# Performance work log

Hardware: AMD Instinct MI355X
Metric: run time of the kernel (lower is better)

Reference implementation:

```python
import jax, jax.numpy as jnp
import numpy as np

N = 50000
E = 800000
EPS = 1e-16
NEG_SLOPE = 0.2

def setup_inputs() -> dict:
    key = jax.random.key(0)
    ks = jax.random.split(key, 10)
    s = lambda fan: 1.0 / np.sqrt(fan)
    return {
        "x": jax.random.normal(ks[0], (N, 128), dtype=jnp.float32),
        "edge_index": jax.random.randint(ks[1], (2, E), 0, N, dtype=jnp.int64),
        "W1": jax.random.normal(ks[2], (128, 4 * 32), dtype=jnp.float32) * s(128),
        "att_src1": jax.random.normal(ks[3], (4, 32), dtype=jnp.float32) * s(32),
        "att_dst1": jax.random.normal(ks[4], (4, 32), dtype=jnp.float32) * s(32),
        "b1": jnp.zeros((128,), dtype=jnp.float32),
        "W2": jax.random.normal(ks[5], (128, 2), dtype=jnp.float32) * s(128),
        "att_src2": jax.random.normal(ks[6], (1, 2), dtype=jnp.float32) * s(2),
        "att_dst2": jax.random.normal(ks[7], (1, 2), dtype=jnp.float32) * s(2),
        "b2": jnp.zeros((2,), dtype=jnp.float32),
    }

def _gat_conv(x, src, dst, W, att_src, att_dst, bias, heads, out_ch, concat):
    n = x.shape[0]
    h = (x @ W).reshape(n, heads, out_ch)                      # [N,H,C]
    a_src = jnp.sum(h * att_src[None], axis=-1)                # [N,H]
    a_dst = jnp.sum(h * att_dst[None], axis=-1)                # [N,H]
    e = jax.nn.leaky_relu(a_src[src] + a_dst[dst], NEG_SLOPE)  # [Etot,H]
    # segment softmax over incoming edges per destination node
    m = jax.ops.segment_max(e, dst, num_segments=n)            # [N,H]
    m = jnp.where(jnp.isfinite(m), m, 0.0)
    ex = jnp.exp(e - m[dst])
    denom = jax.ops.segment_sum(ex, dst, num_segments=n)       # [N,H]
    alpha = ex / (denom[dst] + EPS)                            # [Etot,H]
    out = jax.ops.segment_sum(alpha[:, :, None] * h[src], dst, num_segments=n)  # [N,H,C]
    if concat:
        out = out.reshape(n, heads * out_ch)
    else:
        out = out.mean(axis=1)
    return out + bias

def reference(x, edge_index, W1, att_src1, att_dst1, b1, W2, att_src2, att_dst2, b2):
    n = x.shape[0]
    # PyG GATConv adds self-loops by default
    loops = jnp.arange(n, dtype=edge_index.dtype)
    src = jnp.concatenate([edge_index[0], loops])
    dst = jnp.concatenate([edge_index[1], loops])
    # dropout is identity at inference
    h = jax.nn.elu(_gat_conv(x, src, dst, W1, att_src1, att_dst1, b1, 4, 32, True))
    h = _gat_conv(h, src, dst, W2, att_src2, att_dst2, b2, 1, 2, False)
    return jax.nn.log_softmax(h, axis=1)
```

## Files before the change

### kernel.cpp

```cpp
#include <hip/hip_runtime.h>
#include <hip/hip_bf16.h>

#define NN 50000
#define EE 800000
#define CAP 64
#define CSTRIDE 16
#define NEG_SLOPE 0.2f
#define EPSF 1e-16f
#define BUILD_BLOCKS 4096
#define GEMM_BLOCKS ((NN + 63) / 64)
#define NPAIRS (EE / 2)

typedef unsigned int uint32;
typedef __attribute__((ext_vector_type(8))) short short8;
typedef __attribute__((ext_vector_type(4))) float floatx4;

__device__ __forceinline__ unsigned short f2bf(float f) {
  unsigned int u = __float_as_uint(f);
  unsigned int r = (u + 0x7fffu + ((u >> 16) & 1u)) >> 16;
  return (unsigned short)r;
}
__device__ __forceinline__ float bf_lo(uint32 v) { return __uint_as_float(v << 16); }
__device__ __forceinline__ float bf_hi(uint32 v) { return __uint_as_float(v & 0xffff0000u); }

__device__ __forceinline__ void do_build(int b, const int* __restrict__ ei,
                                         int* __restrict__ counts,
                                         int* __restrict__ csr) {
  const int range = b & 7;
  const int lo = range * (NN / 8);
  const int hi = lo + (NN / 8);
  const int group = b >> 3;
  const int tid0 = group * 256 + threadIdx.x;
  const int stride = (BUILD_BLOCKS >> 3) * 256;

  {
    int n = lo + tid0;
    if (n < hi) csr[n * CAP] = n;
  }

  const int2* __restrict__ dst2 = (const int2*)(ei + EE);
  const int2* __restrict__ src2 = (const int2*)(ei);
  for (int p = tid0; p < NPAIRS; p += stride) {
    int2 d2 = dst2[p];
    int2 s2 = src2[p];
    if (d2.x >= lo && d2.x < hi) {
      int r = atomicAdd(&counts[d2.x * CSTRIDE], 1);
      if (r < CAP) csr[d2.x * CAP + r] = s2.x;
    }
    if (d2.y >= lo && d2.y < hi) {
      int r = atomicAdd(&counts[d2.y * CSTRIDE], 1);
      if (r < CAP) csr[d2.y * CAP + r] = s2.y;
    }
  }
}

__device__ __forceinline__ void do_gemm_tile(
    int tile, const float* __restrict__ x, const unsigned short* __restrict__ Wt,
    const float* __restrict__ att_src1, const float* __restrict__ att_dst1,
    uint32* __restrict__ h1b, float* __restrict__ as1, float* __restrict__ ad1) {
  const int t    = threadIdx.x;
  const int wave = t >> 6;
  const int lane = t & 63;
  const int quad = lane >> 4;
  const int col  = lane & 15;
  const int nodeBase = tile * 64 + wave * 16;

  floatx4 acc[8];
  #pragma unroll
  for (int i = 0; i < 8; i++) acc[i] = (floatx4){0.f, 0.f, 0.f, 0.f};

  int mread = nodeBase + col; if (mread >= NN) mread = NN - 1;
  const float* __restrict__ xrow = x + (size_t)mread * 128 + quad * 8;
  const unsigned short* __restrict__ bbase = Wt + col * 128 + quad * 8;

  #pragma unroll
  for (int ks = 0; ks < 4; ks++) {
    float4 a0 = *(const float4*)(xrow + ks * 32);
    float4 a1 = *(const float4*)(xrow + ks * 32 + 4);
    union { short8 v; unsigned short u[8]; } af;
    af.u[0] = f2bf(a0.x); af.u[1] = f2bf(a0.y);
    af.u[2] = f2bf(a0.z); af.u[3] = f2bf(a0.w);
    af.u[4] = f2bf(a1.x); af.u[5] = f2bf(a1.y);
    af.u[6] = f2bf(a1.z); af.u[7] = f2bf(a1.w);
    #pragma unroll
    for (int tt = 0; tt < 8; tt++) {
      short8 bf = *(const short8*)(bbase + tt * 16 * 128 + ks * 32);
      acc[tt] = __builtin_amdgcn_mfma_f32_16x16x32_bf16(af.v, bf, acc[tt], 0, 0, 0);
    }
  }

  float asv[8], adv[8];
  #pragma unroll
  for (int tt = 0; tt < 8; tt++) {
    asv[tt] = att_src1[tt * 16 + col];
    adv[tt] = att_dst1[tt * 16 + col];
  }

  #pragma unroll
  for (int r = 0; r < 4; r++) {
    const int gn = nodeBase + quad * 4 + r;
    const bool live = (gn < NN);
    #pragma unroll
    for (int tt = 0; tt < 8; tt++) {
      float v = acc[tt][r];
      float w = __shfl_xor(v, 1, 64);
      if (live && ((col & 1) == 0)) {
        uint32 pk = (uint32)f2bf(v) | ((uint32)f2bf(w) << 16);
        h1b[(size_t)gn * 64 + tt * 8 + (col >> 1)] = pk;
      }
    }
    #pragma unroll
    for (int h = 0; h < 4; h++) {
      float ps = acc[2 * h][r] * asv[2 * h] + acc[2 * h + 1][r] * asv[2 * h + 1];
      float pd = acc[2 * h][r] * adv[2 * h] + acc[2 * h + 1][r] * adv[2 * h + 1];
      #pragma unroll
      for (int off = 1; off < 16; off <<= 1) {
        ps += __shfl_xor(ps, off, 64);
        pd += __shfl_xor(pd, off, 64);
      }
      if (live && col == 0) {
        as1[gn * 4 + h] = ps;
        ad1[gn * 4 + h] = pd;
      }
    }
  }
}

__global__ __launch_bounds__(256) void prep_zero_k(
    const float* __restrict__ W1, unsigned short* __restrict__ Wt,
    int* __restrict__ counts) {
  const int step = gridDim.x * 256;
  const int t0 = blockIdx.x * 256 + threadIdx.x;
  for (int i = t0; i < NN * CSTRIDE; i += step)
    counts[i] = ((i & (CSTRIDE - 1)) == 0) ? 1 : 0;
  for (int i = t0; i < 128 * 128; i += step) {
    int k = i >> 7, c = i & 127;
    Wt[c * 128 + k] = f2bf(W1[i]);
  }
}

__global__ __launch_bounds__(256) void work_k(
    const int* __restrict__ ei, int* __restrict__ counts, int* __restrict__ csr,
    const float* __restrict__ x, const unsigned short* __restrict__ Wt,
    const float* __restrict__ att_src1, const float* __restrict__ att_dst1,
    uint32* __restrict__ h1b, float* __restrict__ as1, float* __restrict__ ad1) {
  const int b = blockIdx.x;
  if (b < BUILD_BLOCKS) {
    do_build(b, ei, counts, csr);
  } else {
    do_gemm_tile(b - BUILD_BLOCKS, x, Wt, att_src1, att_dst1, h1b, as1, ad1);
  }
}

__global__ __launch_bounds__(256) void agg1_k(
    const int* __restrict__ counts, const int* __restrict__ csr,
    const uint32* __restrict__ h1b, const float* __restrict__ as1,
    const float* __restrict__ ad1, const float* __restrict__ b1,
    const float* __restrict__ W2, const float* __restrict__ att_src2,
    const float* __restrict__ att_dst2, float4* __restrict__ rec) {
  __shared__ float part[2][3][64];
  const int lane = threadIdx.x & 63;
  const int wv   = threadIdx.x >> 6;
  const int nl   = wv >> 1;
  const int w    = wv & 1;
  const int hd   = lane >> 4;
  const int n = __builtin_amdgcn_readfirstlane(blockIdx.x * 2 + nl);

  int cnt = counts[n * CSTRIDE];
  cnt = __builtin_amdgcn_readfirstlane(cnt < CAP ? cnt : CAP);
  const int half = (cnt + 1) >> 1;
  const int jbeg = w ? half : 0;
  const int jend = w ? cnt : half;
  const int* __restrict__ row = csr + n * CAP;
  const float adv = ad1[n * 4 + hd];

  float den = 0.f, accx = 0.f, accy = 0.f;
  int j = jbeg;
  for (; j + 3 < jend; j += 4) {
    int s0 = row[j], s1 = row[j + 1], s2 = row[j + 2], s3 = row[j + 3];
    float e0 = as1[s0 * 4 + hd] + adv;
    float e1 = as1[s1 * 4 + hd] + adv;
    float e2 = as1[s2 * 4 + hd] + adv;
    float e3 = as1[s3 * 4 + hd] + adv;
    uint32 v0 = h1b[s0 * 64 + lane];
    uint32 v1 = h1b[s1 * 64 + lane];
    uint32 v2 = h1b[s2 * 64 + lane];
    uint32 v3 = h1b[s3 * 64 + lane];
    e0 = (e0 > 0.f) ? e0 : NEG_SLOPE * e0;
    e1 = (e1 > 0.f) ? e1 : NEG_SLOPE * e1;
    e2 = (e2 > 0.f) ? e2 : NEG_SLOPE * e2;
    e3 = (e3 > 0.f) ? e3 : NEG_SLOPE * e3;
    float x0 = __expf(e0), x1 = __expf(e1), x2 = __expf(e2), x3 = __expf(e3);
    den += (x0 + x1) + (x2 + x3);
    accx = fmaf(x0, bf_lo(v0), accx);
    accy = fmaf(x0, bf_hi(v0), accy);
    accx = fmaf(x1, bf_lo(v1), accx);
    accy = fmaf(x1, bf_hi(v1), accy);
    accx = fmaf(x2, bf_lo(v2), accx);
    accy = fmaf(x2, bf_hi(v2), accy);
    accx = fmaf(x3, bf_lo(v3), accx);
    accy = fmaf(x3, bf_hi(v3), accy);
  }
  for (; j < jend; j++) {
    int s = row[j];
    float e = as1[s * 4 + hd] + adv;
    e = (e > 0.f) ? e : NEG_SLOPE * e;
    float ex = __expf(e);
    uint32 v = h1b[s * 64 + lane];
    den += ex;
    accx = fmaf(ex, bf_lo(v), accx);
    accy = fmaf(ex, bf_hi(v), accy);
  }

  if (w == 1) {
    part[nl][0][lane] = den;
    part[nl][1][lane] = accx;
    part[nl][2][lane] = accy;
  }
  __syncthreads();
  if (w == 1) return;
  den  += part[nl][0][lane];
  accx += part[nl][1][lane];
  accy += part[nl][2][lane];

  float inv = 1.f / (den + EPSF);
  float2 bb = ((const float2*)b1)[lane];
  float ox = accx * inv + bb.x;
  float oy = accy * inv + bb.y;
  ox = (ox > 0.f) ? ox : (__expf(ox) - 1.f);
  oy = (oy > 0.f) ? oy : (__expf(oy) - 1.f);

  float4 wq = ((const float4*)W2)[lane];
  float p0 = ox * wq.x + oy * wq.z;
  float p1 = ox * wq.y + oy * wq.w;
  #pragma unroll
  for (int off = 32; off; off >>= 1) {
    p0 += __shfl_xor(p0, off, 64);
    p1 += __shfl_xor(p1, off, 64);
  }
  if (lane == 0) {
    rec[n] = make_float4(p0, p1,
                         p0 * att_src2[0] + p1 * att_src2[1],
                         p0 * att_dst2[0] + p1 * att_dst2[1]);
  }
}

__global__ __launch_bounds__(256) void agg2_k(
    const int* __restrict__ counts, const int* __restrict__ csr,
    const float4* __restrict__ rec, const float* __restrict__ b2,
    float* __restrict__ out) {
  int i = blockIdx.x * 256 + threadIdx.x;
  if (i >= NN * 8) return;
  int n = i >> 3;
  int sub = i & 7;
  const float adv = rec[n].w;
  int cnt = counts[n * CSTRIDE];
  cnt = cnt < CAP ? cnt : CAP;
  const int* __restrict__ row = csr + n * CAP;

  float den = 0.f, a0 = 0.f, a1 = 0.f;
  for (int j = sub; j < cnt; j += 8) {
    int s = row[j];
    float4 rs = rec[s];
    float e = rs.z + adv;
    e = (e > 0.f) ? e : NEG_SLOPE * e;
    float ex = __expf(e);
    den += ex;
    a0 = fmaf(ex, rs.x, a0);
    a1 = fmaf(ex, rs.y, a1);
  }
  #pragma unroll
  for (int off = 4; off; off >>= 1) {
    den += __shfl_down(den, off, 8);
    a0  += __shfl_down(a0, off, 8);
    a1  += __shfl_down(a1, off, 8);
  }
  if (sub == 0) {
    float inv = 1.f / (den + EPSF);
    float o0 = a0 * inv + b2[0];
    float o1 = a1 * inv + b2[1];
    float mx = fmaxf(o0, o1);
    float lse = mx + __logf(__expf(o0 - mx) + __expf(o1 - mx));
    *(float2*)&out[n * 2] = make_float2(o0 - lse, o1 - lse);
  }
}

extern "C" void kernel_launch(void* const* d_in, const int* in_sizes, int n_in,
                              void* d_out, int out_size, void* d_ws, size_t ws_size,
                              hipStream_t stream) {
  const float* x        = (const float*)d_in[0];
  const int*   ei       = (const int*)d_in[1];
  const float* W1       = (const float*)d_in[2];
  const float* att_src1 = (const float*)d_in[3];
  const float* att_dst1 = (const float*)d_in[4];
  const float* b1       = (const float*)d_in[5];
  const float* W2       = (const float*)d_in[6];
  const float* att_src2 = (const float*)d_in[7];
  const float* att_dst2 = (const float*)d_in[8];
  const float* b2       = (const float*)d_in[9];
  float* out = (float*)d_out;

  char* p = (char*)d_ws;
  auto alloc = [&](size_t bytes) {
    char* r = p;
    p += (bytes + 255) & ~size_t(255);
    return r;
  };
  uint32* h1b  = (uint32*)alloc(sizeof(uint32) * NN * 64);
  float* as1   = (float*)alloc(sizeof(float) * NN * 4);
  float* ad1   = (float*)alloc(sizeof(float) * NN * 4);
  float4* rec  = (float4*)alloc(sizeof(float4) * NN);
  int*   counts = (int*)alloc(sizeof(int) * NN * CSTRIDE);
  int*   csr   = (int*)alloc(sizeof(int) * NN * CAP);
  unsigned short* Wt = (unsigned short*)alloc(sizeof(unsigned short) * 128 * 128);

  prep_zero_k<<<512, 256, 0, stream>>>(W1, Wt, counts);
  work_k<<<BUILD_BLOCKS + GEMM_BLOCKS, 256, 0, stream>>>(
      ei, counts, csr, x, Wt, att_src1, att_dst1, h1b, as1, ad1);
  agg1_k<<<NN / 2, 256, 0, stream>>>(counts, csr, h1b, as1, ad1, b1, W2,
                                     att_src2, att_dst2, rec);
  agg2_k<<<(NN * 8 + 255) / 256, 256, 0, stream>>>(counts, csr, rec, b2, out);
}
```

Baseline: 208.1 us.

## Split fused build/GEMM kernel and use one wave per node in aggregation

The combined work kernel that ran CSR build blocks and GEMM tiles side by side is split into two separate launches, so the two jobs no longer overlap. The layer-1 aggregation now gives each node a single wave instead of splitting its edges across two waves with a shared-memory reduction and block barrier. This drops the LDS traffic and __syncthreads and halves the waves per node, but it serialises the build and GEMM phases, adds a launch, and lengthens each wave's edge loop.

```diff
diff --git a/kernel.cpp b/kernel.cpp
--- a/kernel.cpp
+++ b/kernel.cpp
@@ -23,9 +23,23 @@
 __device__ __forceinline__ float bf_lo(uint32 v) { return __uint_as_float(v << 16); }
 __device__ __forceinline__ float bf_hi(uint32 v) { return __uint_as_float(v & 0xffff0000u); }
 
-__device__ __forceinline__ void do_build(int b, const int* __restrict__ ei,
-                                         int* __restrict__ counts,
-                                         int* __restrict__ csr) {
+__global__ __launch_bounds__(256) void prep_zero_k(
+    const float* __restrict__ W1, unsigned short* __restrict__ Wt,
+    int* __restrict__ counts) {
+  const int step = gridDim.x * 256;
+  const int t0 = blockIdx.x * 256 + threadIdx.x;
+  for (int i = t0; i < NN * CSTRIDE; i += step)
+    counts[i] = ((i & (CSTRIDE - 1)) == 0) ? 1 : 0;
+  for (int i = t0; i < 128 * 128; i += step) {
+    int k = i >> 7, c = i & 127;
+    Wt[c * 128 + k] = f2bf(W1[i]);
+  }
+}
+
+__global__ __launch_bounds__(256) void build_k(
+    const int* __restrict__ ei, int* __restrict__ counts,
+    int* __restrict__ csr) {
+  const int b = blockIdx.x;
   const int range = b & 7;
   const int lo = range * (NN / 8);
   const int hi = lo + (NN / 8);
@@ -54,10 +68,11 @@
   }
 }
 
-__device__ __forceinline__ void do_gemm_tile(
-    int tile, const float* __restrict__ x, const unsigned short* __restrict__ Wt,
+__global__ __launch_bounds__(256) void gemm_k(
+    const float* __restrict__ x, const unsigned short* __restrict__ Wt,
     const float* __restrict__ att_src1, const float* __restrict__ att_dst1,
     uint32* __restrict__ h1b, float* __restrict__ as1, float* __restrict__ ad1) {
+  const int tile = blockIdx.x;
   const int t    = threadIdx.x;
   const int wave = t >> 6;
   const int lane = t & 63;
@@ -126,57 +141,25 @@
   }
 }
 
-__global__ __launch_bounds__(256) void prep_zero_k(
-    const float* __restrict__ W1, unsigned short* __restrict__ Wt,
-    int* __restrict__ counts) {
-  const int step = gridDim.x * 256;
-  const int t0 = blockIdx.x * 256 + threadIdx.x;
-  for (int i = t0; i < NN * CSTRIDE; i += step)
-    counts[i] = ((i & (CSTRIDE - 1)) == 0) ? 1 : 0;
-  for (int i = t0; i < 128 * 128; i += step) {
-    int k = i >> 7, c = i & 127;
-    Wt[c * 128 + k] = f2bf(W1[i]);
-  }
-}
-
-__global__ __launch_bounds__(256) void work_k(
-    const int* __restrict__ ei, int* __restrict__ counts, int* __restrict__ csr,
-    const float* __restrict__ x, const unsigned short* __restrict__ Wt,
-    const float* __restrict__ att_src1, const float* __restrict__ att_dst1,
-    uint32* __restrict__ h1b, float* __restrict__ as1, float* __restrict__ ad1) {
-  const int b = blockIdx.x;
-  if (b < BUILD_BLOCKS) {
-    do_build(b, ei, counts, csr);
-  } else {
-    do_gemm_tile(b - BUILD_BLOCKS, x, Wt, att_src1, att_dst1, h1b, as1, ad1);
-  }
-}
-
 __global__ __launch_bounds__(256) void agg1_k(
     const int* __restrict__ counts, const int* __restrict__ csr,
     const uint32* __restrict__ h1b, const float* __restrict__ as1,
     const float* __restrict__ ad1, const float* __restrict__ b1,
     const float* __restrict__ W2, const float* __restrict__ att_src2,
     const float* __restrict__ att_dst2, float4* __restrict__ rec) {
-  __shared__ float part[2][3][64];
   const int lane = threadIdx.x & 63;
-  const int wv   = threadIdx.x >> 6;
-  const int nl   = wv >> 1;
-  const int w    = wv & 1;
-  const int hd   = lane >> 4;
-  const int n = __builtin_amdgcn_readfirstlane(blockIdx.x * 2 + nl);
+  const int wv = threadIdx.x >> 6;
+  const int hd = lane >> 4;
+  const int n = __builtin_amdgcn_readfirstlane(blockIdx.x * 4 + wv);
 
   int cnt = counts[n * CSTRIDE];
   cnt = __builtin_amdgcn_readfirstlane(cnt < CAP ? cnt : CAP);
-  const int half = (cnt + 1) >> 1;
-  const int jbeg = w ? half : 0;
-  const int jend = w ? cnt : half;
   const int* __restrict__ row = csr + n * CAP;
   const float adv = ad1[n * 4 + hd];
 
   float den = 0.f, accx = 0.f, accy = 0.f;
-  int j = jbeg;
-  for (; j + 3 < jend; j += 4) {
+  int j = 0;
+  for (; j + 3 < cnt; j += 4) {
     int s0 = row[j], s1 = row[j + 1], s2 = row[j + 2], s3 = row[j + 3];
     float e0 = as1[s0 * 4 + hd] + adv;
     float e1 = as1[s1 * 4 + hd] + adv;
@@ -201,7 +184,7 @@
     accx = fmaf(x3, bf_lo(v3), accx);
     accy = fmaf(x3, bf_hi(v3), accy);
   }
-  for (; j < jend; j++) {
+  for (; j < cnt; j++) {
     int s = row[j];
     float e = as1[s * 4 + hd] + adv;
     e = (e > 0.f) ? e : NEG_SLOPE * e;
@@ -211,17 +194,6 @@
     accx = fmaf(ex, bf_lo(v), accx);
     accy = fmaf(ex, bf_hi(v), accy);
   }
-
-  if (w == 1) {
-    part[nl][0][lane] = den;
-    part[nl][1][lane] = accx;
-    part[nl][2][lane] = accy;
-  }
-  __syncthreads();
-  if (w == 1) return;
-  den  += part[nl][0][lane];
-  accx += part[nl][1][lane];
-  accy += part[nl][2][lane];
 
   float inv = 1.f / (den + EPSF);
   float2 bb = ((const float2*)b1)[lane];
@@ -315,9 +287,10 @@
   unsigned short* Wt = (unsigned short*)alloc(sizeof(unsigned short) * 128 * 128);
 
   prep_zero_k<<<512, 256, 0, stream>>>(W1, Wt, counts);
-  work_k<<<BUILD_BLOCKS + GEMM_BLOCKS, 256, 0, stream>>>(
-      ei, counts, csr, x, Wt, att_src1, att_dst1, h1b, as1, ad1);
-  agg1_k<<<NN / 2, 256, 0, stream>>>(counts, csr, h1b, as1, ad1, b1, W2,
+  build_k<<<BUILD_BLOCKS, 256, 0, stream>>>(ei, counts, csr);
+  gemm_k<<<GEMM_BLOCKS, 256, 0, stream>>>(x, Wt, att_src1, att_dst1,
+                                          h1b, as1, ad1);
+  agg1_k<<<NN / 4, 256, 0, stream>>>(counts, csr, h1b, as1, ad1, b1, W2,
                                      att_src2, att_dst2, rec);
   agg2_k<<<(NN * 8 + 255) / 256, 256, 0, stream>>>(counts, csr, rec, b2, out);
 }
```

Measured after the change: 192.5 us. 1.08x faster.
